# Kernel optimization log

Measured on AMD Instinct MI355X. Metric: run time of the kernel, lower is better.

The kernel has to match this reference:

```python
import jax, jax.numpy as jnp
from jax import lax
import numpy as np

OBJECT_W, BCE_W, DICE_W = 2.0, 5.0, 5.0
B, N, M, C = 8, 128, 32, 65536


def setup_inputs() -> dict:
    key = jax.random.key(0)
    k1, k2, k3 = jax.random.split(key, 3)
    objectness = jax.random.normal(k1, (B, N), jnp.float32)
    pred_masks = jax.random.normal(k2, (B, N, C), jnp.float32)
    gt_masks = jax.random.randint(k3, (B, M, C), 0, 2).astype(jnp.float32)
    return {"objectness": objectness, "pred_masks": pred_masks, "gt_masks": gt_masks}


def _cost_matrices(objectness, pred, gt):
    # BCE-with-logits vs all-ones target: log(1+exp(-x)) = softplus(-x)
    # BCE-with-logits vs all-zeros target: softplus(x)
    sp_pos = jax.nn.softplus(-pred)                       # [B,N,C]
    sp_neg = jax.nn.softplus(pred)                        # [B,N,C]
    # einsum('nc,mc->nm', pos, t) + einsum('nc,mc->nm', neg, 1-t), batched.
    # neg @ (1-t) = neg.sum(c) - neg @ t (avoids materializing 1-t).
    bce = (jnp.einsum('bnc,bmc->bnm', sp_pos, gt)
           + sp_neg.sum(-1)[:, :, None]
           - jnp.einsum('bnc,bmc->bnm', sp_neg, gt)) / pred.shape[-1]
    s = jax.nn.sigmoid(pred)
    numerator = 2.0 * jnp.einsum('bnc,bmc->bnm', s, gt)
    denominator = s.sum(-1)[:, :, None] + gt.sum(-1)[:, None, :]
    dice = 1.0 - (numerator + 1.0) / (denominator + 1.0)
    obj = -jax.nn.sigmoid(objectness)[:, :, None]         # [B,N,1]
    return OBJECT_W * obj + BCE_W * bce + DICE_W * dice    # [B,N,M]


def _lsap(cost):
    """Jonker-Volgenant shortest-augmenting-path LSAP (scipy algorithm).
    cost: [R, C] with R <= C. Returns col4row [R] int32: column per row."""
    R, Cn = cost.shape
    BIG = jnp.float32(1e30)

    def outer(cur_row, carry):
        u, v, row4col, col4row = carry
        shortest = jnp.full((Cn,), BIG, jnp.float32)
        path = jnp.full((Cn,), -1, jnp.int32)
        SR = jnp.zeros((R,), bool)
        SC = jnp.zeros((Cn,), bool)

        def sp_cond(s):
            return s[6] < 0

        def sp_body(s):
            i, shortest, path, SR, SC, minVal, sink = s
            SR = SR.at[i].set(True)
            d = minVal + cost[i] - u[i] - v
            better = (d < shortest) & (~SC)
            shortest = jnp.where(better, d, shortest)
            path = jnp.where(better, i, path)
            masked = jnp.where(SC, BIG, shortest)
            j = jnp.argmin(masked).astype(jnp.int32)
            minVal = masked[j]
            SC = SC.at[j].set(True)
            nxt = row4col[j]
            sink = jnp.where(nxt == -1, j, jnp.int32(-1))
            i = jnp.where(nxt == -1, i, nxt)
            return (i, shortest, path, SR, SC, minVal, sink)

        init = (cur_row.astype(jnp.int32), shortest, path, SR, SC,
                jnp.float32(0.0), jnp.int32(-1))
        i, shortest, path, SR, SC, minVal, sink = lax.while_loop(sp_cond, sp_body, init)

        # dual updates (scipy rectangular_lsap)
        u = u.at[cur_row].add(minVal)
        extra = SR & (jnp.arange(R) != cur_row)
        sp_at_col = shortest[jnp.clip(col4row, 0, Cn - 1)]
        u = jnp.where(extra, u + minVal - sp_at_col, u)
        v = jnp.where(SC, v - (minVal - shortest), v)

        # augment along path
        def aug_cond(s):
            return ~s[3]

        def aug_body(s):
            j, row4col, col4row, done = s
            i = path[j]
            row4col = row4col.at[j].set(i)
            tmp = col4row[i]
            col4row = col4row.at[i].set(j)
            done = (i == cur_row)
            return (tmp, row4col, col4row, done)

        _, row4col, col4row, _ = lax.while_loop(
            aug_cond, aug_body, (sink, row4col, col4row, jnp.array(False)))
        return (u, v, row4col, col4row)

    carry = (jnp.zeros((R,), jnp.float32), jnp.zeros((Cn,), jnp.float32),
             jnp.full((Cn,), -1, jnp.int32), jnp.full((R,), -1, jnp.int32))
    u, v, row4col, col4row = lax.fori_loop(0, R, outer, carry)
    return col4row


def reference(objectness, pred_masks, gt_masks):
    cost = _cost_matrices(objectness, pred_masks, gt_masks)   # [B,N,M]
    # scipy lsap on [N,M] then sort by target == solving on cost.T [M,N]:
    # indices[b, m] = matched query index for target m.
    indices = jax.vmap(_lsap)(jnp.transpose(cost, (0, 2, 1)))  # [B,M]
    return cost, indices
```

## Files before the change

### kernel.cpp

```cpp
#include <hip/hip_runtime.h>
#include <hip/hip_bf16.h>

#define LOG2E 1.4426950408889634f
#define LN2   0.6931471805599453f

typedef __attribute__((ext_vector_type(8))) short short8;
typedef __attribute__((ext_vector_type(4))) float f32x4;

#define B_ 8
#define N_ 128
#define M_ 32
#define C_ 65536
#define KCHUNKS 64
#define KC (C_ / KCHUNKS)
#define BK 64
#define AST 72

__device__ __forceinline__ unsigned short f2bf(float f) {
  unsigned u = __builtin_bit_cast(unsigned, f);
  u += 0x7fffu + ((u >> 16) & 1u);
  return (unsigned short)(u >> 16);
}
__device__ __forceinline__ unsigned pack_rne(float lo, float hi) {
  return (unsigned)f2bf(lo) | ((unsigned)f2bf(hi) << 16);
}
__device__ __forceinline__ unsigned pack_trunc(float lo, float hi) {
  unsigned ul = __builtin_bit_cast(unsigned, lo);
  unsigned uh = __builtin_bit_cast(unsigned, hi);
  return (uh & 0xFFFF0000u) | (ul >> 16);
}

__global__ __launch_bounds__(256, 2) void cost_partial_kernel(
    const float* __restrict__ pred, const float* __restrict__ gt,
    float* __restrict__ xg_part, float* __restrict__ sg_part,
    float* __restrict__ sp_part, float* __restrict__ ss_part,
    float* __restrict__ gts_part)
{
  __shared__ unsigned short As[256 * AST];
  __shared__ unsigned short Bt[32 * AST];
  const int kc = blockIdx.x, b = blockIdx.y;
  const int tid = threadIdx.x;
  const int grp = tid >> 4, gl = tid & 15;
  const int grow = tid >> 3, gh = tid & 7;
  const int wave = tid >> 6, lane = tid & 63;
  const int quad = lane >> 4, lcol = lane & 15;
  const int c0 = kc * KC;
  const int slab = kc * B_ + b;

  const float* predB = pred + (size_t)b * N_ * C_ + c0;
  const float* gtB   = gt   + (size_t)b * M_ * C_ + (size_t)grow * C_ + c0;

  float spr[8], sr[8], gtacc = 0.f;
#pragma unroll
  for (int r = 0; r < 8; ++r) { spr[r] = 0.f; sr[r] = 0.f; }

  f32x4 acc[4][2];
#pragma unroll
  for (int rt = 0; rt < 4; ++rt)
#pragma unroll
    for (int ct = 0; ct < 2; ++ct)
      acc[rt][ct] = (f32x4){0.f, 0.f, 0.f, 0.f};

  for (int ks = 0; ks < KC / BK; ++ks) {
    const int cb = ks * BK;
    float4 p[8];
#pragma unroll
    for (int r = 0; r < 8; ++r)
      p[r] = *(const float4*)(predB + (size_t)(r * 16 + grp) * C_ + cb + gl * 4);
    float4 g0 = *(const float4*)(gtB + cb + gh * 4);
    float4 g1 = *(const float4*)(gtB + cb + (gh + 8) * 4);

#pragma unroll
    for (int r = 0; r < 8; ++r) {
      const int row = r * 16 + grp;
      float xs[4] = {p[r].x, p[r].y, p[r].z, p[r].w};
      float ss[4];
#pragma unroll
      for (int e = 0; e < 4; ++e) {
        float x = xs[e];
        float t = fminf(fmaxf(x * LOG2E, -80.f), 80.f);
        float e2 = __builtin_amdgcn_exp2f(t);
        float z = 1.f + e2;
        float s = e2 * __builtin_amdgcn_rcpf(z);
        spr[r] += __builtin_amdgcn_logf(z) * LN2;
        sr[r]  += s;
        ss[e] = s;
      }
      *(uint2*)&As[row * AST + gl * 4] =
          (uint2){pack_rne(xs[0], xs[1]), pack_rne(xs[2], xs[3])};
      *(uint2*)&As[(N_ + row) * AST + gl * 4] =
          (uint2){pack_rne(ss[0], ss[1]), pack_rne(ss[2], ss[3])};
    }
    gtacc += g0.x + g0.y + g0.z + g0.w + g1.x + g1.y + g1.z + g1.w;
    *(uint2*)&Bt[grow * AST + gh * 4] =
        (uint2){pack_trunc(g0.x, g0.y), pack_trunc(g0.z, g0.w)};
    *(uint2*)&Bt[grow * AST + (gh + 8) * 4] =
        (uint2){pack_trunc(g1.x, g1.y), pack_trunc(g1.z, g1.w)};
    __syncthreads();

#pragma unroll
    for (int k0 = 0; k0 < BK; k0 += 32) {
      const int koff = k0 + quad * 8;
      short8 bf0 = *(const short8*)&Bt[lcol * AST + koff];
      short8 bf1 = *(const short8*)&Bt[(16 + lcol) * AST + koff];
#pragma unroll
      for (int rt = 0; rt < 4; ++rt) {
        short8 af = *(const short8*)&As[(wave * 64 + rt * 16 + lcol) * AST + koff];
        acc[rt][0] = __builtin_amdgcn_mfma_f32_16x16x32_bf16(af, bf0, acc[rt][0], 0, 0, 0);
        acc[rt][1] = __builtin_amdgcn_mfma_f32_16x16x32_bf16(af, bf1, acc[rt][1], 0, 0, 0);
      }
    }
    __syncthreads();
  }

#pragma unroll
  for (int r = 0; r < 8; ++r) {
    float v1 = spr[r], v2 = sr[r];
#pragma unroll
    for (int off = 1; off < 16; off <<= 1) {
      v1 += __shfl_xor(v1, off);
      v2 += __shfl_xor(v2, off);
    }
    if (gl == 0) {
      sp_part[slab * N_ + r * 16 + grp] = v1;
      ss_part[slab * N_ + r * 16 + grp] = v2;
    }
  }
  gtacc += __shfl_xor(gtacc, 1);
  gtacc += __shfl_xor(gtacc, 2);
  gtacc += __shfl_xor(gtacc, 4);
  if (gh == 0) gts_part[slab * M_ + grow] = gtacc;

#pragma unroll
  for (int rt = 0; rt < 4; ++rt)
#pragma unroll
    for (int ct = 0; ct < 2; ++ct)
#pragma unroll
      for (int reg = 0; reg < 4; ++reg) {
        int orow = wave * 64 + rt * 16 + quad * 4 + reg;
        int ocol = ct * 16 + lcol;
        float v = acc[rt][ct][reg];
        if (orow < N_) xg_part[(slab * N_ + orow) * M_ + ocol] = v;
        else           sg_part[(slab * N_ + (orow - N_)) * M_ + ocol] = v;
      }
}

__global__ void finalize_kernel(const float* __restrict__ obj,
    const float* __restrict__ xg_part, const float* __restrict__ sg_part,
    const float* __restrict__ sp_part, const float* __restrict__ ss_part,
    const float* __restrict__ gts_part, float* __restrict__ cost)
{
  int idx = blockIdx.x * blockDim.x + threadIdx.x;
  int b = idx >> 12;
  int n = (idx >> 5) & 127;
  int m = idx & 31;
  float xa = 0.f, sa = 0.f, spa = 0.f, ssa = 0.f, ga = 0.f;
#pragma unroll 4
  for (int kc = 0; kc < KCHUNKS; ++kc) {
    int slab = kc * B_ + b;
    xa  += xg_part[(slab * N_ + n) * M_ + m];
    sa  += sg_part[(slab * N_ + n) * M_ + m];
    spa += sp_part[slab * N_ + n];
    ssa += ss_part[slab * N_ + n];
    ga  += gts_part[slab * M_ + m];
  }
  float o = obj[b * N_ + n];
  float t = fminf(fmaxf(o * LOG2E, -80.f), 80.f);
  float e2 = __builtin_amdgcn_exp2f(t);
  float sig = e2 * __builtin_amdgcn_rcpf(1.f + e2);
  float bce = (spa - xa) * (1.0f / (float)C_);
  float dice = 1.f - (2.f * sa + 1.f) / (ssa + ga + 1.f);
  cost[idx] = -2.f * sig + 5.f * bce + 5.f * dice;
}

#define BIGF 1e30f

__device__ __forceinline__ float wave_min_all(float x) {
  const int BI = __builtin_bit_cast(int, BIGF);
  int v = __builtin_bit_cast(int, x);
#define MIN_STEP(ctrl)                                                        \
  {                                                                           \
    int t_ = __builtin_amdgcn_update_dpp(BI, v, ctrl, 0xf, 0xf, false);       \
    v = __builtin_bit_cast(int, fminf(__builtin_bit_cast(float, v),           \
                                      __builtin_bit_cast(float, t_)));        \
  }
  MIN_STEP(0x111)
  MIN_STEP(0x112)
  MIN_STEP(0x114)
  MIN_STEP(0x118)
  MIN_STEP(0x142)
  MIN_STEP(0x143)
#undef MIN_STEP
  return __builtin_bit_cast(float, __builtin_amdgcn_readlane(v, 63));
}

__device__ __forceinline__ float rdlane_f(float x, int l) {
  return __builtin_bit_cast(float, __builtin_amdgcn_readlane(__builtin_bit_cast(int, x), l));
}

__global__ __launch_bounds__(64) void lsap_kernel(const float* __restrict__ cost,
                                                  float* __restrict__ out)
{
  const int b = blockIdx.x;
  const int lane = threadIdx.x;
  __shared__ float cTs[M_ * 129];

#pragma unroll 4
  for (int t = 0; t < 16; ++t) {
    int e = t * 256 + lane * 4;
    float4 v4 = *(const float4*)&cost[b * 4096 + e];
    int n = e >> 5, m = e & 31;
    cTs[(m + 0) * 129 + n] = v4.x;
    cTs[(m + 1) * 129 + n] = v4.y;
    cTs[(m + 2) * 129 + n] = v4.z;
    cTs[(m + 3) * 129 + n] = v4.w;
  }
  __syncthreads();

  float u_reg = 0.f;
  int c4r = -1;
  float v0 = 0.f, v1 = 0.f;
  int r40 = -1, r41 = -1;

  for (int cur = 0; cur < M_; ++cur) {
    float sh0 = BIGF, sh1 = BIGF;
    int p0 = -1, p1 = -1;
    bool sc0 = false, sc1 = false;
    unsigned srmask = 0u;
    int i = cur, sink = -1;
    float minVal = 0.f;

    while (sink < 0) {
      srmask |= 1u << i;
      float ui = rdlane_f(u_reg, i);
      float cc0 = cTs[i * 129 + 2 * lane];
      float cc1 = cTs[i * 129 + 2 * lane + 1];
      float d0 = ((minVal + cc0) - ui) - v0;
      float d1 = ((minVal + cc1) - ui) - v1;
      if (!sc0 && d0 < sh0) { sh0 = d0; p0 = i; }
      if (!sc1 && d1 < sh1) { sh1 = d1; p1 = i; }
      float m0 = sc0 ? BIGF : sh0;
      float m1 = sc1 ? BIGF : sh1;
      float mv = wave_min_all(fminf(m0, m1));
      unsigned long long bl0 = __ballot(m0 == mv);
      unsigned long long bl1 = __ballot(m1 == mv);
      int j0 = bl0 ? 2 * (int)__builtin_ctzll(bl0) : 0x7fffffff;
      int j1 = bl1 ? 2 * (int)__builtin_ctzll(bl1) + 1 : 0x7fffffff;
      int j = j0 < j1 ? j0 : j1;
      minVal = mv;
      if (lane == (j >> 1)) { if (j & 1) sc1 = true; else sc0 = true; }
      int nxt = __builtin_amdgcn_readlane((j & 1) ? r41 : r40, j >> 1);
      if (nxt < 0) sink = j; else i = nxt;
    }

    int jj = c4r < 0 ? 0 : c4r;
    float g0 = __shfl(sh0, jj >> 1);
    float g1 = __shfl(sh1, jj >> 1);
    float sj = (jj & 1) ? g1 : g0;
    if (lane < M_) {
      if (lane == cur) u_reg += minVal;
      else if ((srmask >> lane) & 1u) u_reg += minVal - sj;
    }
    if (sc0) v0 -= minVal - sh0;
    if (sc1) v1 -= minVal - sh1;

    int j = sink;
    while (true) {
      int i2 = __builtin_amdgcn_readlane((j & 1) ? p1 : p0, j >> 1);
      if (lane == (j >> 1)) { if (j & 1) r41 = i2; else r40 = i2; }
      int tmp = __builtin_amdgcn_readlane(c4r, i2);
      if (lane == i2) c4r = j;
      if (i2 == cur) break;
      j = tmp;
    }
  }
  if (lane < M_) out[b * M_ + lane] = (float)c4r;
}

extern "C" void kernel_launch(void* const* d_in, const int* in_sizes, int n_in,
                              void* d_out, int out_size, void* d_ws, size_t ws_size,
                              hipStream_t stream)
{
  const float* obj  = (const float*)d_in[0];
  const float* pred = (const float*)d_in[1];
  const float* gt   = (const float*)d_in[2];
  float* out = (float*)d_out;

  float* xg_part  = (float*)d_ws;
  float* sg_part  = xg_part + (size_t)KCHUNKS * B_ * N_ * M_;
  float* sp_part  = sg_part + (size_t)KCHUNKS * B_ * N_ * M_;
  float* ss_part  = sp_part + (size_t)KCHUNKS * B_ * N_;
  float* gts_part = ss_part + (size_t)KCHUNKS * B_ * N_;

  cost_partial_kernel<<<dim3(KCHUNKS, B_), 256, 0, stream>>>(
      pred, gt, xg_part, sg_part, sp_part, ss_part, gts_part);
  finalize_kernel<<<dim3(32768 / 256), 256, 0, stream>>>(
      obj, xg_part, sg_part, sp_part, ss_part, gts_part, out);
  lsap_kernel<<<dim3(B_), 64, 0, stream>>>(out, out + 32768);
}
```

Before: 569.3 us.

## Feed MFMA A operands directly from registers and stage GT tile once

The cost-partial kernel no longer stages the transformed pred values through shared memory. Each lane loads its own 8-element slice of pred, computes softplus and sigmoid, and packs bf16 fragments straight into MFMA A registers. The whole GT chunk is staged to LDS once per block, so the per-step syncs are gone. KCHUNKS doubles to 128 and launch bounds rise to 4 blocks per CU, which gives more blocks but also doubles the partial buffers that finalize must reduce.

```diff
diff --git a/kernel.cpp b/kernel.cpp
--- a/kernel.cpp
+++ b/kernel.cpp
@@ -11,137 +11,137 @@
 #define N_ 128
 #define M_ 32
 #define C_ 65536
-#define KCHUNKS 64
+#define KCHUNKS 128
 #define KC (C_ / KCHUNKS)
-#define BK 64
-#define AST 72
+#define BST (KC + 8)
 
 __device__ __forceinline__ unsigned short f2bf(float f) {
   unsigned u = __builtin_bit_cast(unsigned, f);
   u += 0x7fffu + ((u >> 16) & 1u);
   return (unsigned short)(u >> 16);
 }
-__device__ __forceinline__ unsigned pack_rne(float lo, float hi) {
-  return (unsigned)f2bf(lo) | ((unsigned)f2bf(hi) << 16);
-}
-__device__ __forceinline__ unsigned pack_trunc(float lo, float hi) {
-  unsigned ul = __builtin_bit_cast(unsigned, lo);
-  unsigned uh = __builtin_bit_cast(unsigned, hi);
-  return (uh & 0xFFFF0000u) | (ul >> 16);
-}
-
-__global__ __launch_bounds__(256, 2) void cost_partial_kernel(
+
+__global__ __launch_bounds__(256, 4) void cost_partial_kernel(
     const float* __restrict__ pred, const float* __restrict__ gt,
     float* __restrict__ xg_part, float* __restrict__ sg_part,
     float* __restrict__ sp_part, float* __restrict__ ss_part,
     float* __restrict__ gts_part)
 {
-  __shared__ unsigned short As[256 * AST];
-  __shared__ unsigned short Bt[32 * AST];
+  __shared__ unsigned short Bt[M_ * BST];
   const int kc = blockIdx.x, b = blockIdx.y;
   const int tid = threadIdx.x;
-  const int grp = tid >> 4, gl = tid & 15;
-  const int grow = tid >> 3, gh = tid & 7;
-  const int wave = tid >> 6, lane = tid & 63;
+  const int g = tid >> 6, lane = tid & 63;
   const int quad = lane >> 4, lcol = lane & 15;
+  const int slab = kc * B_ + b;
   const int c0 = kc * KC;
-  const int slab = kc * B_ + b;
-
-  const float* predB = pred + (size_t)b * N_ * C_ + c0;
-  const float* gtB   = gt   + (size_t)b * M_ * C_ + (size_t)grow * C_ + c0;
-
-  float spr[8], sr[8], gtacc = 0.f;
-#pragma unroll
-  for (int r = 0; r < 8; ++r) { spr[r] = 0.f; sr[r] = 0.f; }
-
-  f32x4 acc[4][2];
-#pragma unroll
-  for (int rt = 0; rt < 4; ++rt)
-#pragma unroll
-    for (int ct = 0; ct < 2; ++ct)
-      acc[rt][ct] = (f32x4){0.f, 0.f, 0.f, 0.f};
-
-  for (int ks = 0; ks < KC / BK; ++ks) {
-    const int cb = ks * BK;
-    float4 p[8];
-#pragma unroll
-    for (int r = 0; r < 8; ++r)
-      p[r] = *(const float4*)(predB + (size_t)(r * 16 + grp) * C_ + cb + gl * 4);
-    float4 g0 = *(const float4*)(gtB + cb + gh * 4);
-    float4 g1 = *(const float4*)(gtB + cb + (gh + 8) * 4);
-
-#pragma unroll
-    for (int r = 0; r < 8; ++r) {
-      const int row = r * 16 + grp;
-      float xs[4] = {p[r].x, p[r].y, p[r].z, p[r].w};
-      float ss[4];
-#pragma unroll
-      for (int e = 0; e < 4; ++e) {
+
+  {
+    const int row = tid >> 3, gh = tid & 7;
+    const float* gp = gt + (size_t)b * M_ * C_ + (size_t)row * C_ + c0 + gh * 64;
+    float ga = 0.f;
+#pragma unroll
+    for (int i = 0; i < 16; ++i) {
+      float4 v = *(const float4*)(gp + i * 4);
+      ga += v.x + v.y + v.z + v.w;
+      unsigned lo = (__builtin_bit_cast(unsigned, v.y) & 0xFFFF0000u) |
+                    (__builtin_bit_cast(unsigned, v.x) >> 16);
+      unsigned hi = (__builtin_bit_cast(unsigned, v.w) & 0xFFFF0000u) |
+                    (__builtin_bit_cast(unsigned, v.z) >> 16);
+      *(uint2*)&Bt[row * BST + gh * 64 + i * 4] = (uint2){lo, hi};
+    }
+    ga += __shfl_xor(ga, 1);
+    ga += __shfl_xor(ga, 2);
+    ga += __shfl_xor(ga, 4);
+    if (gh == 0) gts_part[slab * M_ + row] = ga;
+  }
+  __syncthreads();
+
+  const float* pA = pred + (size_t)b * N_ * C_ + (size_t)(g * 32) * C_ + c0;
+  const float* rowp0 = pA + (size_t)lcol * C_;
+  const float* rowp1 = pA + (size_t)(16 + lcol) * C_;
+
+  f32x4 ax[2][2], as_[2][2];
+#pragma unroll
+  for (int rt = 0; rt < 2; ++rt)
+#pragma unroll
+    for (int ct = 0; ct < 2; ++ct) {
+      ax[rt][ct] = (f32x4){0.f, 0.f, 0.f, 0.f};
+      as_[rt][ct] = (f32x4){0.f, 0.f, 0.f, 0.f};
+    }
+  float sp0 = 0.f, sp1 = 0.f, ss0 = 0.f, ss1 = 0.f;
+
+  for (int ks = 0; ks < KC; ks += 32) {
+    const int kq = ks + quad * 8;
+    float4 a0 = *(const float4*)(rowp0 + kq);
+    float4 a1 = *(const float4*)(rowp0 + kq + 4);
+    float4 a2 = *(const float4*)(rowp1 + kq);
+    float4 a3 = *(const float4*)(rowp1 + kq + 4);
+
+    short8 xf0, sf0, xf1, sf1;
+    {
+      float xs[8] = {a0.x, a0.y, a0.z, a0.w, a1.x, a1.y, a1.z, a1.w};
+#pragma unroll
+      for (int e = 0; e < 8; ++e) {
         float x = xs[e];
         float t = fminf(fmaxf(x * LOG2E, -80.f), 80.f);
         float e2 = __builtin_amdgcn_exp2f(t);
         float z = 1.f + e2;
         float s = e2 * __builtin_amdgcn_rcpf(z);
-        spr[r] += __builtin_amdgcn_logf(z) * LN2;
-        sr[r]  += s;
-        ss[e] = s;
+        sp0 += __builtin_amdgcn_logf(z) * LN2;
+        ss0 += s;
+        xf0[e] = (short)f2bf(x);
+        sf0[e] = (short)f2bf(s);
       }
-      *(uint2*)&As[row * AST + gl * 4] =
-          (uint2){pack_rne(xs[0], xs[1]), pack_rne(xs[2], xs[3])};
-      *(uint2*)&As[(N_ + row) * AST + gl * 4] =
-          (uint2){pack_rne(ss[0], ss[1]), pack_rne(ss[2], ss[3])};
-    }
-    gtacc += g0.x + g0.y + g0.z + g0.w + g1.x + g1.y + g1.z + g1.w;
-    *(uint2*)&Bt[grow * AST + gh * 4] =
-        (uint2){pack_trunc(g0.x, g0.y), pack_trunc(g0.z, g0.w)};
-    *(uint2*)&Bt[grow * AST + (gh + 8) * 4] =
-        (uint2){pack_trunc(g1.x, g1.y), pack_trunc(g1.z, g1.w)};
-    __syncthreads();
-
-#pragma unroll
-    for (int k0 = 0; k0 < BK; k0 += 32) {
-      const int koff = k0 + quad * 8;
-      short8 bf0 = *(const short8*)&Bt[lcol * AST + koff];
-      short8 bf1 = *(const short8*)&Bt[(16 + lcol) * AST + koff];
-#pragma unroll
-      for (int rt = 0; rt < 4; ++rt) {
-        short8 af = *(const short8*)&As[(wave * 64 + rt * 16 + lcol) * AST + koff];
-        acc[rt][0] = __builtin_amdgcn_mfma_f32_16x16x32_bf16(af, bf0, acc[rt][0], 0, 0, 0);
-        acc[rt][1] = __builtin_amdgcn_mfma_f32_16x16x32_bf16(af, bf1, acc[rt][1], 0, 0, 0);
+    }
+    {
+      float xs[8] = {a2.x, a2.y, a2.z, a2.w, a3.x, a3.y, a3.z, a3.w};
+#pragma unroll
+      for (int e = 0; e < 8; ++e) {
+        float x = xs[e];
+        float t = fminf(fmaxf(x * LOG2E, -80.f), 80.f);
+        float e2 = __builtin_amdgcn_exp2f(t);
+        float z = 1.f + e2;
+        float s = e2 * __builtin_amdgcn_rcpf(z);
+        sp1 += __builtin_amdgcn_logf(z) * LN2;
+        ss1 += s;
+        xf1[e] = (short)f2bf(x);
+        sf1[e] = (short)f2bf(s);
       }
     }
-    __syncthreads();
-  }
-
-#pragma unroll
-  for (int r = 0; r < 8; ++r) {
-    float v1 = spr[r], v2 = sr[r];
-#pragma unroll
-    for (int off = 1; off < 16; off <<= 1) {
-      v1 += __shfl_xor(v1, off);
-      v2 += __shfl_xor(v2, off);
-    }
-    if (gl == 0) {
-      sp_part[slab * N_ + r * 16 + grp] = v1;
-      ss_part[slab * N_ + r * 16 + grp] = v2;
-    }
-  }
-  gtacc += __shfl_xor(gtacc, 1);
-  gtacc += __shfl_xor(gtacc, 2);
-  gtacc += __shfl_xor(gtacc, 4);
-  if (gh == 0) gts_part[slab * M_ + grow] = gtacc;
-
-#pragma unroll
-  for (int rt = 0; rt < 4; ++rt)
+
+    short8 b0 = *(const short8*)&Bt[lcol * BST + kq];
+    short8 b1 = *(const short8*)&Bt[(16 + lcol) * BST + kq];
+
+    ax[0][0] = __builtin_amdgcn_mfma_f32_16x16x32_bf16(xf0, b0, ax[0][0], 0, 0, 0);
+    ax[0][1] = __builtin_amdgcn_mfma_f32_16x16x32_bf16(xf0, b1, ax[0][1], 0, 0, 0);
+    ax[1][0] = __builtin_amdgcn_mfma_f32_16x16x32_bf16(xf1, b0, ax[1][0], 0, 0, 0);
+    ax[1][1] = __builtin_amdgcn_mfma_f32_16x16x32_bf16(xf1, b1, ax[1][1], 0, 0, 0);
+    as_[0][0] = __builtin_amdgcn_mfma_f32_16x16x32_bf16(sf0, b0, as_[0][0], 0, 0, 0);
+    as_[0][1] = __builtin_amdgcn_mfma_f32_16x16x32_bf16(sf0, b1, as_[0][1], 0, 0, 0);
+    as_[1][0] = __builtin_amdgcn_mfma_f32_16x16x32_bf16(sf1, b0, as_[1][0], 0, 0, 0);
+    as_[1][1] = __builtin_amdgcn_mfma_f32_16x16x32_bf16(sf1, b1, as_[1][1], 0, 0, 0);
+  }
+
+  sp0 += __shfl_xor(sp0, 16); sp0 += __shfl_xor(sp0, 32);
+  sp1 += __shfl_xor(sp1, 16); sp1 += __shfl_xor(sp1, 32);
+  ss0 += __shfl_xor(ss0, 16); ss0 += __shfl_xor(ss0, 32);
+  ss1 += __shfl_xor(ss1, 16); ss1 += __shfl_xor(ss1, 32);
+  if (quad == 0) {
+    const int r0 = g * 32 + lcol;
+    sp_part[slab * N_ + r0] = sp0;      sp_part[slab * N_ + r0 + 16] = sp1;
+    ss_part[slab * N_ + r0] = ss0;      ss_part[slab * N_ + r0 + 16] = ss1;
+  }
+
+#pragma unroll
+  for (int rt = 0; rt < 2; ++rt)
 #pragma unroll
     for (int ct = 0; ct < 2; ++ct)
 #pragma unroll
       for (int reg = 0; reg < 4; ++reg) {
-        int orow = wave * 64 + rt * 16 + quad * 4 + reg;
-        int ocol = ct * 16 + lcol;
-        float v = acc[rt][ct][reg];
-        if (orow < N_) xg_part[(slab * N_ + orow) * M_ + ocol] = v;
-        else           sg_part[(slab * N_ + (orow - N_)) * M_ + ocol] = v;
+        const int r = g * 32 + rt * 16 + quad * 4 + reg;
+        const int c = ct * 16 + lcol;
+        xg_part[((size_t)slab * N_ + r) * M_ + c] = ax[rt][ct][reg];
+        sg_part[((size_t)slab * N_ + r) * M_ + c] = as_[rt][ct][reg];
       }
 }
 
@@ -155,11 +155,11 @@
   int n = (idx >> 5) & 127;
   int m = idx & 31;
   float xa = 0.f, sa = 0.f, spa = 0.f, ssa = 0.f, ga = 0.f;
-#pragma unroll 4
+#pragma unroll 8
   for (int kc = 0; kc < KCHUNKS; ++kc) {
     int slab = kc * B_ + b;
-    xa  += xg_part[(slab * N_ + n) * M_ + m];
-    sa  += sg_part[(slab * N_ + n) * M_ + m];
+    xa  += xg_part[((size_t)slab * N_ + n) * M_ + m];
+    sa  += sg_part[((size_t)slab * N_ + n) * M_ + m];
     spa += sp_part[slab * N_ + n];
     ssa += ss_part[slab * N_ + n];
     ga  += gts_part[slab * M_ + m];
```

After: 647.1 us. +13.7%, slower.

## Recompute sigmoid from bf16 A-fragments in MFMA loop, halve LDS, double K-chunks

Applied to the files above, without the earlier changes.

The sigmoid tile is no longer stored in shared memory. Each wave recomputes the sigmoid from the bf16 logits it loads for the MFMA, which halves the A-tile LDS footprint and raises launch bounds to four blocks per CU. KCHUNKS doubles to 128 for more blocks, and finalize unrolls deeper to match. The cost is duplicated transcendental work in the inner loop, sigmoid computed from bf16-rounded inputs (a small precision change), and twice the partial-sum traffic into finalize.

```diff
diff --git a/kernel.cpp b/kernel.cpp
--- a/kernel.cpp
+++ b/kernel.cpp
@@ -11,7 +11,7 @@
 #define N_ 128
 #define M_ 32
 #define C_ 65536
-#define KCHUNKS 64
+#define KCHUNKS 128
 #define KC (C_ / KCHUNKS)
 #define BK 64
 #define AST 72
@@ -29,23 +29,26 @@
   unsigned uh = __builtin_bit_cast(unsigned, hi);
   return (uh & 0xFFFF0000u) | (ul >> 16);
 }
-
-__global__ __launch_bounds__(256, 2) void cost_partial_kernel(
+__device__ __forceinline__ float bf2f(short h) {
+  return __builtin_bit_cast(float, ((unsigned)(unsigned short)h) << 16);
+}
+
+__global__ __launch_bounds__(256, 4) void cost_partial_kernel(
     const float* __restrict__ pred, const float* __restrict__ gt,
     float* __restrict__ xg_part, float* __restrict__ sg_part,
     float* __restrict__ sp_part, float* __restrict__ ss_part,
     float* __restrict__ gts_part)
 {
-  __shared__ unsigned short As[256 * AST];
-  __shared__ unsigned short Bt[32 * AST];
+  __shared__ unsigned short As[N_ * AST];
+  __shared__ unsigned short Bt[M_ * AST];
   const int kc = blockIdx.x, b = blockIdx.y;
   const int tid = threadIdx.x;
   const int grp = tid >> 4, gl = tid & 15;
   const int grow = tid >> 3, gh = tid & 7;
-  const int wave = tid >> 6, lane = tid & 63;
+  const int g = tid >> 6, lane = tid & 63;
   const int quad = lane >> 4, lcol = lane & 15;
+  const int slab = kc * B_ + b;
   const int c0 = kc * KC;
-  const int slab = kc * B_ + b;
 
   const float* predB = pred + (size_t)b * N_ * C_ + c0;
   const float* gtB   = gt   + (size_t)b * M_ * C_ + (size_t)grow * C_ + c0;
@@ -54,12 +57,14 @@
 #pragma unroll
   for (int r = 0; r < 8; ++r) { spr[r] = 0.f; sr[r] = 0.f; }
 
-  f32x4 acc[4][2];
-#pragma unroll
-  for (int rt = 0; rt < 4; ++rt)
-#pragma unroll
-    for (int ct = 0; ct < 2; ++ct)
-      acc[rt][ct] = (f32x4){0.f, 0.f, 0.f, 0.f};
+  f32x4 ax[2][2], as_[2][2];
+#pragma unroll
+  for (int rt = 0; rt < 2; ++rt)
+#pragma unroll
+    for (int ct = 0; ct < 2; ++ct) {
+      ax[rt][ct]  = (f32x4){0.f, 0.f, 0.f, 0.f};
+      as_[rt][ct] = (f32x4){0.f, 0.f, 0.f, 0.f};
+    }
 
   for (int ks = 0; ks < KC / BK; ++ks) {
     const int cb = ks * BK;
@@ -74,22 +79,17 @@
     for (int r = 0; r < 8; ++r) {
       const int row = r * 16 + grp;
       float xs[4] = {p[r].x, p[r].y, p[r].z, p[r].w};
-      float ss[4];
 #pragma unroll
       for (int e = 0; e < 4; ++e) {
         float x = xs[e];
         float t = fminf(fmaxf(x * LOG2E, -80.f), 80.f);
         float e2 = __builtin_amdgcn_exp2f(t);
         float z = 1.f + e2;
-        float s = e2 * __builtin_amdgcn_rcpf(z);
         spr[r] += __builtin_amdgcn_logf(z) * LN2;
-        sr[r]  += s;
-        ss[e] = s;
+        sr[r]  += e2 * __builtin_amdgcn_rcpf(z);
       }
       *(uint2*)&As[row * AST + gl * 4] =
           (uint2){pack_rne(xs[0], xs[1]), pack_rne(xs[2], xs[3])};
-      *(uint2*)&As[(N_ + row) * AST + gl * 4] =
-          (uint2){pack_rne(ss[0], ss[1]), pack_rne(ss[2], ss[3])};
     }
     gtacc += g0.x + g0.y + g0.z + g0.w + g1.x + g1.y + g1.z + g1.w;
     *(uint2*)&Bt[grow * AST + gh * 4] =
@@ -101,13 +101,23 @@
 #pragma unroll
     for (int k0 = 0; k0 < BK; k0 += 32) {
       const int koff = k0 + quad * 8;
-      short8 bf0 = *(const short8*)&Bt[lcol * AST + koff];
-      short8 bf1 = *(const short8*)&Bt[(16 + lcol) * AST + koff];
-#pragma unroll
-      for (int rt = 0; rt < 4; ++rt) {
-        short8 af = *(const short8*)&As[(wave * 64 + rt * 16 + lcol) * AST + koff];
-        acc[rt][0] = __builtin_amdgcn_mfma_f32_16x16x32_bf16(af, bf0, acc[rt][0], 0, 0, 0);
-        acc[rt][1] = __builtin_amdgcn_mfma_f32_16x16x32_bf16(af, bf1, acc[rt][1], 0, 0, 0);
+      short8 b0 = *(const short8*)&Bt[lcol * AST + koff];
+      short8 b1 = *(const short8*)&Bt[(16 + lcol) * AST + koff];
+#pragma unroll
+      for (int rt = 0; rt < 2; ++rt) {
+        short8 xf = *(const short8*)&As[(g * 32 + rt * 16 + lcol) * AST + koff];
+        short8 sf;
+#pragma unroll
+        for (int e = 0; e < 8; ++e) {
+          float x = bf2f(xf[e]);
+          float t = fminf(fmaxf(x * LOG2E, -80.f), 80.f);
+          float e2 = __builtin_amdgcn_exp2f(t);
+          sf[e] = (short)f2bf(e2 * __builtin_amdgcn_rcpf(1.f + e2));
+        }
+        ax[rt][0]  = __builtin_amdgcn_mfma_f32_16x16x32_bf16(xf, b0, ax[rt][0], 0, 0, 0);
+        ax[rt][1]  = __builtin_amdgcn_mfma_f32_16x16x32_bf16(xf, b1, ax[rt][1], 0, 0, 0);
+        as_[rt][0] = __builtin_amdgcn_mfma_f32_16x16x32_bf16(sf, b0, as_[rt][0], 0, 0, 0);
+        as_[rt][1] = __builtin_amdgcn_mfma_f32_16x16x32_bf16(sf, b1, as_[rt][1], 0, 0, 0);
       }
     }
     __syncthreads();
@@ -132,16 +142,15 @@
   if (gh == 0) gts_part[slab * M_ + grow] = gtacc;
 
 #pragma unroll
-  for (int rt = 0; rt < 4; ++rt)
+  for (int rt = 0; rt < 2; ++rt)
 #pragma unroll
     for (int ct = 0; ct < 2; ++ct)
 #pragma unroll
       for (int reg = 0; reg < 4; ++reg) {
-        int orow = wave * 64 + rt * 16 + quad * 4 + reg;
-        int ocol = ct * 16 + lcol;
-        float v = acc[rt][ct][reg];
-        if (orow < N_) xg_part[(slab * N_ + orow) * M_ + ocol] = v;
-        else           sg_part[(slab * N_ + (orow - N_)) * M_ + ocol] = v;
+        const int r = g * 32 + rt * 16 + quad * 4 + reg;
+        const int c = ct * 16 + lcol;
+        xg_part[((size_t)slab * N_ + r) * M_ + c] = ax[rt][ct][reg];
+        sg_part[((size_t)slab * N_ + r) * M_ + c] = as_[rt][ct][reg];
       }
 }
 
@@ -155,11 +164,11 @@
   int n = (idx >> 5) & 127;
   int m = idx & 31;
   float xa = 0.f, sa = 0.f, spa = 0.f, ssa = 0.f, ga = 0.f;
-#pragma unroll 4
+#pragma unroll 8
   for (int kc = 0; kc < KCHUNKS; ++kc) {
     int slab = kc * B_ + b;
-    xa  += xg_part[(slab * N_ + n) * M_ + m];
-    sa  += sg_part[(slab * N_ + n) * M_ + m];
+    xa  += xg_part[((size_t)slab * N_ + n) * M_ + m];
+    sa  += sg_part[((size_t)slab * N_ + n) * M_ + m];
     spa += sp_part[slab * N_ + n];
     ssa += ss_part[slab * N_ + n];
     ga  += gts_part[slab * M_ + m];
```

Measured after the change: 644.6 us. 1.13x slower.

## Split cost kernel over row tiles with double-buffered LDS staging

Applied to the files above, without the earlier changes.

Each block of the cost partial-sum kernel now covers 32 pred rows (grid becomes KCHUNKS x 4 x B) instead of all 128, and KCHUNKS drops from 64 to 32. Shared memory is double-buffered: the next K-slice is loaded from global and converted to bf16 while MFMAs run on the current slice, removing one barrier per iteration. The aim is higher occupancy (launch bounds 4) and overlap of global loads with compute. The cost is that gt is reloaded by four blocks per chunk, and finalize now reduces fewer partials using smaller blocks.

```diff
diff --git a/kernel.cpp b/kernel.cpp
--- a/kernel.cpp
+++ b/kernel.cpp
@@ -11,9 +11,10 @@
 #define N_ 128
 #define M_ 32
 #define C_ 65536
-#define KCHUNKS 64
+#define KCHUNKS 32
 #define KC (C_ / KCHUNKS)
 #define BK 64
+#define NK (KC / BK)
 #define AST 72
 
 __device__ __forceinline__ unsigned short f2bf(float f) {
@@ -30,136 +31,143 @@
   return (uh & 0xFFFF0000u) | (ul >> 16);
 }
 
-__global__ __launch_bounds__(256, 2) void cost_partial_kernel(
+__global__ __launch_bounds__(256, 4) void cost_partial_kernel(
     const float* __restrict__ pred, const float* __restrict__ gt,
     float* __restrict__ xg_part, float* __restrict__ sg_part,
     float* __restrict__ sp_part, float* __restrict__ ss_part,
     float* __restrict__ gts_part)
 {
-  __shared__ unsigned short As[256 * AST];
-  __shared__ unsigned short Bt[32 * AST];
-  const int kc = blockIdx.x, b = blockIdx.y;
+  __shared__ unsigned short Asx[2][32 * AST];
+  __shared__ unsigned short Ass[2][32 * AST];
+  __shared__ unsigned short Btb[2][32 * AST];
+  const int kc = blockIdx.x, rt = blockIdx.y, b = blockIdx.z;
   const int tid = threadIdx.x;
-  const int grp = tid >> 4, gl = tid & 15;
-  const int grow = tid >> 3, gh = tid & 7;
+  const int strow = tid >> 3, h = tid & 7;
   const int wave = tid >> 6, lane = tid & 63;
   const int quad = lane >> 4, lcol = lane & 15;
+  const int mat = wave >> 1;
+  const int rhalf = (wave & 1) * 16;
+  const int slab = kc * B_ + b;
   const int c0 = kc * KC;
-  const int slab = kc * B_ + b;
-
-  const float* predB = pred + (size_t)b * N_ * C_ + c0;
-  const float* gtB   = gt   + (size_t)b * M_ * C_ + (size_t)grow * C_ + c0;
-
-  float spr[8], sr[8], gtacc = 0.f;
-#pragma unroll
-  for (int r = 0; r < 8; ++r) { spr[r] = 0.f; sr[r] = 0.f; }
-
-  f32x4 acc[4][2];
-#pragma unroll
-  for (int rt = 0; rt < 4; ++rt)
-#pragma unroll
-    for (int ct = 0; ct < 2; ++ct)
-      acc[rt][ct] = (f32x4){0.f, 0.f, 0.f, 0.f};
-
-  for (int ks = 0; ks < KC / BK; ++ks) {
-    const int cb = ks * BK;
-    float4 p[8];
-#pragma unroll
-    for (int r = 0; r < 8; ++r)
-      p[r] = *(const float4*)(predB + (size_t)(r * 16 + grp) * C_ + cb + gl * 4);
-    float4 g0 = *(const float4*)(gtB + cb + gh * 4);
-    float4 g1 = *(const float4*)(gtB + cb + (gh + 8) * 4);
-
-#pragma unroll
-    for (int r = 0; r < 8; ++r) {
-      const int row = r * 16 + grp;
-      float xs[4] = {p[r].x, p[r].y, p[r].z, p[r].w};
-      float ss[4];
-#pragma unroll
-      for (int e = 0; e < 4; ++e) {
-        float x = xs[e];
-        float t = fminf(fmaxf(x * LOG2E, -80.f), 80.f);
-        float e2 = __builtin_amdgcn_exp2f(t);
-        float z = 1.f + e2;
-        float s = e2 * __builtin_amdgcn_rcpf(z);
-        spr[r] += __builtin_amdgcn_logf(z) * LN2;
-        sr[r]  += s;
-        ss[e] = s;
-      }
-      *(uint2*)&As[row * AST + gl * 4] =
-          (uint2){pack_rne(xs[0], xs[1]), pack_rne(xs[2], xs[3])};
-      *(uint2*)&As[(N_ + row) * AST + gl * 4] =
-          (uint2){pack_rne(ss[0], ss[1]), pack_rne(ss[2], ss[3])};
-    }
-    gtacc += g0.x + g0.y + g0.z + g0.w + g1.x + g1.y + g1.z + g1.w;
-    *(uint2*)&Bt[grow * AST + gh * 4] =
-        (uint2){pack_trunc(g0.x, g0.y), pack_trunc(g0.z, g0.w)};
-    *(uint2*)&Bt[grow * AST + (gh + 8) * 4] =
-        (uint2){pack_trunc(g1.x, g1.y), pack_trunc(g1.z, g1.w)};
+
+  const float* predRow = pred + ((size_t)b * N_ + rt * 32 + strow) * C_ + c0 + h * 4;
+  const float* gtRow   = gt + ((size_t)b * M_ + strow) * C_ + c0 + h * 4;
+
+  float spacc = 0.f, ssacc = 0.f, gtacc = 0.f;
+  f32x4 acc[2];
+  acc[0] = (f32x4){0.f, 0.f, 0.f, 0.f};
+  acc[1] = (f32x4){0.f, 0.f, 0.f, 0.f};
+
+  float4 pp0, pp1, gg0, gg1;
+
+#define LOADK(ks_)                                              \
+  {                                                             \
+    const float* pr_ = predRow + (ks_) * BK;                    \
+    const float* gr_ = gtRow + (ks_) * BK;                      \
+    pp0 = *(const float4*)(pr_);                                \
+    pp1 = *(const float4*)(pr_ + 32);                           \
+    gg0 = *(const float4*)(gr_);                                \
+    gg1 = *(const float4*)(gr_ + 32);                           \
+  }
+
+#define STAGE(buf_)                                                           \
+  {                                                                           \
+    float xs_[8] = {pp0.x, pp0.y, pp0.z, pp0.w, pp1.x, pp1.y, pp1.z, pp1.w};  \
+    float ss_[8];                                                             \
+    _Pragma("unroll") for (int e = 0; e < 8; ++e) {                           \
+      float x_ = xs_[e];                                                      \
+      float t_ = fminf(fmaxf(x_ * LOG2E, -80.f), 80.f);                       \
+      float e2_ = __builtin_amdgcn_exp2f(t_);                                 \
+      float z_ = 1.f + e2_;                                                   \
+      float s_ = e2_ * __builtin_amdgcn_rcpf(z_);                             \
+      spacc += __builtin_amdgcn_logf(z_) * LN2;                               \
+      ssacc += s_;                                                            \
+      ss_[e] = s_;                                                            \
+    }                                                                         \
+    *(uint2*)&Asx[buf_][strow * AST + h * 4] =                                \
+        (uint2){pack_rne(xs_[0], xs_[1]), pack_rne(xs_[2], xs_[3])};          \
+    *(uint2*)&Asx[buf_][strow * AST + h * 4 + 32] =                           \
+        (uint2){pack_rne(xs_[4], xs_[5]), pack_rne(xs_[6], xs_[7])};          \
+    *(uint2*)&Ass[buf_][strow * AST + h * 4] =                                \
+        (uint2){pack_rne(ss_[0], ss_[1]), pack_rne(ss_[2], ss_[3])};          \
+    *(uint2*)&Ass[buf_][strow * AST + h * 4 + 32] =                           \
+        (uint2){pack_rne(ss_[4], ss_[5]), pack_rne(ss_[6], ss_[7])};          \
+    gtacc += gg0.x + gg0.y + gg0.z + gg0.w + gg1.x + gg1.y + gg1.z + gg1.w;   \
+    *(uint2*)&Btb[buf_][strow * AST + h * 4] =                                \
+        (uint2){pack_trunc(gg0.x, gg0.y), pack_trunc(gg0.z, gg0.w)};          \
+    *(uint2*)&Btb[buf_][strow * AST + h * 4 + 32] =                           \
+        (uint2){pack_trunc(gg1.x, gg1.y), pack_trunc(gg1.z, gg1.w)};          \
+  }
+
+  LOADK(0)
+  STAGE(0)
+
+  int cur = 0;
+  for (int ks = 0; ks < NK; ++ks) {
     __syncthreads();
-
+    const bool more = (ks + 1 < NK);
+    if (more) LOADK(ks + 1)
+
+    const unsigned short* Af =
+        (mat ? &Ass[cur][0] : &Asx[cur][0]) + (rhalf + lcol) * AST;
+    const unsigned short* Bf = &Btb[cur][0];
 #pragma unroll
     for (int k0 = 0; k0 < BK; k0 += 32) {
       const int koff = k0 + quad * 8;
-      short8 bf0 = *(const short8*)&Bt[lcol * AST + koff];
-      short8 bf1 = *(const short8*)&Bt[(16 + lcol) * AST + koff];
+      short8 av = *(const short8*)&Af[koff];
+      short8 b0 = *(const short8*)&Bf[lcol * AST + koff];
+      short8 b1 = *(const short8*)&Bf[(16 + lcol) * AST + koff];
+      acc[0] = __builtin_amdgcn_mfma_f32_16x16x32_bf16(av, b0, acc[0], 0, 0, 0);
+      acc[1] = __builtin_amdgcn_mfma_f32_16x16x32_bf16(av, b1, acc[1], 0, 0, 0);
+    }
+    if (more) STAGE(cur ^ 1)
+    cur ^= 1;
+  }
+#undef LOADK
+#undef STAGE
+
+  spacc += __shfl_xor(spacc, 1);
+  spacc += __shfl_xor(spacc, 2);
+  spacc += __shfl_xor(spacc, 4);
+  ssacc += __shfl_xor(ssacc, 1);
+  ssacc += __shfl_xor(ssacc, 2);
+  ssacc += __shfl_xor(ssacc, 4);
+  if (h == 0) {
+    sp_part[slab * N_ + rt * 32 + strow] = spacc;
+    ss_part[slab * N_ + rt * 32 + strow] = ssacc;
+  }
+  if (rt == 0) {
+    gtacc += __shfl_xor(gtacc, 1);
+    gtacc += __shfl_xor(gtacc, 2);
+    gtacc += __shfl_xor(gtacc, 4);
+    if (h == 0) gts_part[slab * M_ + strow] = gtacc;
+  }
+
+  float* dst = mat ? sg_part : xg_part;
 #pragma unroll
-      for (int rt = 0; rt < 4; ++rt) {
-        short8 af = *(const short8*)&As[(wave * 64 + rt * 16 + lcol) * AST + koff];
-        acc[rt][0] = __builtin_amdgcn_mfma_f32_16x16x32_bf16(af, bf0, acc[rt][0], 0, 0, 0);
-        acc[rt][1] = __builtin_amdgcn_mfma_f32_16x16x32_bf16(af, bf1, acc[rt][1], 0, 0, 0);
-      }
-    }
-    __syncthreads();
-  }
-
+  for (int ct = 0; ct < 2; ++ct)
 #pragma unroll
-  for (int r = 0; r < 8; ++r) {
-    float v1 = spr[r], v2 = sr[r];
-#pragma unroll
-    for (int off = 1; off < 16; off <<= 1) {
-      v1 += __shfl_xor(v1, off);
-      v2 += __shfl_xor(v2, off);
-    }
-    if (gl == 0) {
-      sp_part[slab * N_ + r * 16 + grp] = v1;
-      ss_part[slab * N_ + r * 16 + grp] = v2;
-    }
-  }
-  gtacc += __shfl_xor(gtacc, 1);
-  gtacc += __shfl_xor(gtacc, 2);
-  gtacc += __shfl_xor(gtacc, 4);
-  if (gh == 0) gts_part[slab * M_ + grow] = gtacc;
-
-#pragma unroll
-  for (int rt = 0; rt < 4; ++rt)
-#pragma unroll
-    for (int ct = 0; ct < 2; ++ct)
-#pragma unroll
-      for (int reg = 0; reg < 4; ++reg) {
-        int orow = wave * 64 + rt * 16 + quad * 4 + reg;
-        int ocol = ct * 16 + lcol;
-        float v = acc[rt][ct][reg];
-        if (orow < N_) xg_part[(slab * N_ + orow) * M_ + ocol] = v;
-        else           sg_part[(slab * N_ + (orow - N_)) * M_ + ocol] = v;
-      }
-}
-
-__global__ void finalize_kernel(const float* __restrict__ obj,
+    for (int reg = 0; reg < 4; ++reg) {
+      const int r = rt * 32 + rhalf + quad * 4 + reg;
+      dst[((size_t)slab * N_ + r) * M_ + ct * 16 + lcol] = acc[ct][reg];
+    }
+}
+
+__global__ __launch_bounds__(128) void finalize_kernel(const float* __restrict__ obj,
     const float* __restrict__ xg_part, const float* __restrict__ sg_part,
     const float* __restrict__ sp_part, const float* __restrict__ ss_part,
     const float* __restrict__ gts_part, float* __restrict__ cost)
 {
-  int idx = blockIdx.x * blockDim.x + threadIdx.x;
+  int idx = blockIdx.x * 128 + threadIdx.x;
   int b = idx >> 12;
   int n = (idx >> 5) & 127;
   int m = idx & 31;
   float xa = 0.f, sa = 0.f, spa = 0.f, ssa = 0.f, ga = 0.f;
-#pragma unroll 4
+#pragma unroll 8
   for (int kc = 0; kc < KCHUNKS; ++kc) {
     int slab = kc * B_ + b;
-    xa  += xg_part[(slab * N_ + n) * M_ + m];
-    sa  += sg_part[(slab * N_ + n) * M_ + m];
+    xa  += xg_part[((size_t)slab * N_ + n) * M_ + m];
+    sa  += sg_part[((size_t)slab * N_ + n) * M_ + m];
     spa += sp_part[slab * N_ + n];
     ssa += ss_part[slab * N_ + n];
     ga  += gts_part[slab * M_ + m];
@@ -292,9 +300,9 @@
   float* ss_part  = sp_part + (size_t)KCHUNKS * B_ * N_;
   float* gts_part = ss_part + (size_t)KCHUNKS * B_ * N_;
 
-  cost_partial_kernel<<<dim3(KCHUNKS, B_), 256, 0, stream>>>(
+  cost_partial_kernel<<<dim3(KCHUNKS, 4, B_), 256, 0, stream>>>(
       pred, gt, xg_part, sg_part, sp_part, ss_part, gts_part);
-  finalize_kernel<<<dim3(32768 / 256), 256, 0, stream>>>(
+  finalize_kernel<<<dim3(32768 / 128), 128, 0, stream>>>(
       obj, xg_part, sg_part, sp_part, ss_part, gts_part, out);
   lsap_kernel<<<dim3(B_), 64, 0, stream>>>(out, out + 32768);
 }
```

Measured after the change: 575.0 us. About the same (+1.0%).
